# Kernel optimization log

Measured on AMD Instinct MI355X. Metric: run time of the kernel, lower is better.

Reference implementation:

```python
import jax, jax.numpy as jnp
import numpy as np

P_CLASSES = 1024   # num_classes_per_batch
K_SAMP = 4         # num_samples_per_class
MARGIN = 1.0
EPS = 1e-6
EMBED_DIM = 128


def setup_inputs() -> dict:
    key = jax.random.key(0)
    x = jax.random.normal(key, (P_CLASSES * K_SAMP, EMBED_DIM), dtype=jnp.float32)
    return {"x": x}


def reference(x):
    p, k = P_CLASSES, K_SAMP
    n = p * k
    # pairwise distances D[i,j] = sqrt(relu(|xi|^2 - 2 xi.xj + |xj|^2) + eps)
    norms = jnp.sum(x * x, axis=1)
    D = norms[:, None] - 2.0 * (x @ x.T) + norms[None, :]
    D = jnp.sqrt(jax.nn.relu(D) + EPS)  # [n, n]

    # all positive pairs (i<j) within each class, vectorized over classes
    ii, jj = np.triu_indices(k, 1)                      # [m], m = k*(k-1)/2
    c = np.arange(p)
    ri = (c[:, None] * k + ii[None, :]).reshape(-1)     # [P] = [p*m]
    rj = (c[:, None] * k + jj[None, :]).reshape(-1)
    pair_cls = np.repeat(c, len(ii))                    # class of each pair
    col_cls = np.arange(n) // k                         # class of each column
    neg_mask = jnp.asarray(pair_cls[:, None] != col_cls[None, :])  # [P, n]

    # masked logsumexp over negatives from both anchor rows (concat of the
    # two sliced rows in the original code)
    rows = jnp.concatenate([D[ri], D[rj]], axis=1)                 # [P, 2n]
    mask2 = jnp.concatenate([neg_mask, neg_mask], axis=1)
    vals = jnp.where(mask2, MARGIN - rows, -jnp.inf)
    lse = jax.scipy.special.logsumexp(vals, axis=1)                # [P]

    J = lse + D[ri, rj]
    return jnp.mean(jnp.square(jax.nn.relu(J))) / 2.0
```

## Files before the change

kernel.cpp:

```cpp
#include <hip/hip_runtime.h>

#define NROWS 4096
#define DIM 128
#define PCLS 1024
#define NPAIR 6144
#define MARGIN 1.0f
#define EPS 1e-6f
#define LOG2E 1.4426950408889634f
#define NSPLIT 16

typedef __attribute__((ext_vector_type(8))) short bf16x8;
typedef __attribute__((ext_vector_type(4))) float f32x4;

union FragU { uint4 u; bf16x8 v; };

__device__ __forceinline__ unsigned short f2bf(float f) {
    unsigned int b = __float_as_uint(f);
    b = (b + 0x7FFFu + ((b >> 16) & 1u)) >> 16;
    return (unsigned short)b;
}
__device__ __forceinline__ float bf2f(unsigned short u) {
    return __uint_as_float((unsigned int)u << 16);
}

__global__ void prep_kernel(const float* __restrict__ x,
                            unsigned short* __restrict__ xbf,
                            float* __restrict__ norms) {
    int row = blockIdx.x * 4 + (threadIdx.x >> 6);
    int l = threadIdx.x & 63;
    float2 v = *reinterpret_cast<const float2*>(x + row * DIM + 2 * l);
    unsigned int packed = (unsigned int)f2bf(v.x) | ((unsigned int)f2bf(v.y) << 16);
    *reinterpret_cast<unsigned int*>(xbf + row * DIM + 2 * l) = packed;
    float s = v.x * v.x + v.y * v.y;
    #pragma unroll
    for (int m = 1; m < 64; m <<= 1) s += __shfl_xor(s, m, 64);
    if (l == 0) norms[row] = s;
}

__launch_bounds__(512, 4)
__global__ void main_kernel(const unsigned short* __restrict__ xbf,
                            const float* __restrict__ norms,
                            unsigned short* __restrict__ partial,
                            float* __restrict__ posD) {
    __shared__ __align__(16) unsigned short lds[256 * DIM];
    const int t = threadIdx.x;
    const int w = t >> 6;
    const int l = t & 63;
    const int rb = blockIdx.x >> 4;
    const int cs = blockIdx.x & 15;
    const int rbase = rb * 128 + w * 16;
    const int cbase = cs * 256;
    const int lg = l >> 4;
    const int lr = l & 15;

    FragU afr[4];
    const char* abase = (const char*)xbf + (size_t)(rbase + lr) * 256 + lg * 16;
    #pragma unroll
    for (int s = 0; s < 4; ++s)
        afr[s].u = *reinterpret_cast<const uint4*>(abase + s * 64);

    float njv[16];
    #pragma unroll
    for (int tile = 0; tile < 16; ++tile)
        njv[tile] = norms[cbase + tile * 16 + lr];

    float ni[4];
    #pragma unroll
    for (int rr = 0; rr < 4; ++rr)
        ni[rr] = norms[rbase + lg * 4 + rr] + EPS;

    #pragma unroll
    for (int it = 0; it < 8; ++it) {
        int lin = it * 8192 + t * 16;
        int col = lin >> 8;
        int inner = lin & 255;
        uint4 v = *reinterpret_cast<const uint4*>(
            (const char*)xbf + (size_t)(cbase + col) * 256 + inner);
        *reinterpret_cast<uint4*>(
            (char*)lds + col * 256 + (inner ^ ((col & 7) << 4))) = v;
    }

    __syncthreads();

    float accS[4] = {0.f, 0.f, 0.f, 0.f};

    #pragma unroll
    for (int tile = 0; tile < 16; ++tile) {
        const int lcol = tile * 16 + lr;
        const float nj = njv[tile];
        const char* bbase = (const char*)lds + lcol * 256;
        const int xr = (lcol & 7) << 4;
        f32x4 acc = {0.f, 0.f, 0.f, 0.f};
        #pragma unroll
        for (int s = 0; s < 4; ++s) {
            FragU bu;
            int inner = s * 64 + lg * 16;
            bu.u = *reinterpret_cast<const uint4*>(bbase + (inner ^ xr));
            acc = __builtin_amdgcn_mfma_f32_16x16x32_bf16(afr[s].v, bu.v, acc, 0, 0, 0);
        }
        const bool diag = (cbase + tile * 16) == rbase;
        if (!diag) {
            #pragma unroll
            for (int rr = 0; rr < 4; ++rr) {
                float nn = ni[rr] + nj;
                float d2 = fmaf(-2.0f, acc[rr], nn);
                float d = __builtin_amdgcn_sqrtf(fmaxf(d2, EPS));
                accS[rr] += __builtin_amdgcn_exp2f(fmaf(d, -LOG2E, LOG2E));
            }
        } else {
            #pragma unroll
            for (int rr = 0; rr < 4; ++rr) {
                int a = lg * 4 + rr;
                int b = lr;
                float nn = ni[rr] + nj;
                float d2 = fmaf(-2.0f, acc[rr], nn);
                float d = __builtin_amdgcn_sqrtf(fmaxf(d2, EPS));
                float e = __builtin_amdgcn_exp2f(fmaf(d, -LOG2E, LOG2E));
                bool same = (a >> 2) == (b >> 2);
                accS[rr] += same ? 0.f : e;
                if (same && a < b) {
                    int i = a & 3, j = b & 3;
                    int idx = i * (7 - i) / 2 + (j - i - 1);
                    int cls = (rbase + a) >> 2;
                    posD[cls * 6 + idx] = d;
                }
            }
        }
    }
    #pragma unroll
    for (int rr = 0; rr < 4; ++rr) {
        #pragma unroll
        for (int m = 1; m < 16; m <<= 1) accS[rr] += __shfl_xor(accS[rr], m, 64);
    }
    if (lr == 0) {
        #pragma unroll
        for (int rr = 0; rr < 4; ++rr)
            partial[cs * NROWS + rbase + lg * 4 + rr] = f2bf(accS[rr]);
    }
}

__global__ void tail_kernel(const unsigned short* __restrict__ partial,
                            const float* __restrict__ posD,
                            float* __restrict__ out) {
    const int c = threadIdx.x;
    float S[4] = {0.f, 0.f, 0.f, 0.f};
    #pragma unroll
    for (int sp = 0; sp < NSPLIT; ++sp) {
        ushort4 v = *reinterpret_cast<const ushort4*>(partial + sp * NROWS + 4 * c);
        S[0] += bf2f(v.x); S[1] += bf2f(v.y); S[2] += bf2f(v.z); S[3] += bf2f(v.w);
    }
    const int II[6] = {0, 0, 0, 1, 1, 2};
    const int JJ[6] = {1, 2, 3, 2, 3, 3};
    float acc = 0.f;
    #pragma unroll
    for (int p = 0; p < 6; ++p) {
        float d = posD[c * 6 + p];
        float J = __logf(S[II[p]] + S[JJ[p]]) + d;
        float r = fmaxf(J, 0.f);
        acc += r * r;
    }
    #pragma unroll
    for (int m = 1; m < 64; m <<= 1) acc += __shfl_xor(acc, m, 64);
    __shared__ float red[16];
    if ((c & 63) == 0) red[c >> 6] = acc;
    __syncthreads();
    if (c < 64) {
        float v = (c < 16) ? red[c] : 0.f;
        #pragma unroll
        for (int m = 1; m < 16; m <<= 1) v += __shfl_xor(v, m, 64);
        if (c == 0) out[0] = v * (1.0f / (2.0f * (float)NPAIR));
    }
}

extern "C" void kernel_launch(void* const* d_in, const int* in_sizes, int n_in,
                              void* d_out, int out_size, void* d_ws, size_t ws_size,
                              hipStream_t stream) {
    const float* x = (const float*)d_in[0];
    char* ws = (char*)d_ws;
    unsigned short* xbf = (unsigned short*)ws;
    float* norms = (float*)(ws + 1048576);
    unsigned short* partial = (unsigned short*)(ws + 1048576 + 16384);
    float* posD = (float*)(ws + 1048576 + 16384 + 131072);
    float* out = (float*)d_out;

    hipLaunchKernelGGL(prep_kernel, dim3(NROWS / 4), dim3(256), 0, stream, x, xbf, norms);
    hipLaunchKernelGGL(main_kernel, dim3(512), dim3(512), 0, stream, xbf, norms, partial, posD);
    hipLaunchKernelGGL(tail_kernel, dim3(1), dim3(1024), 0, stream, partial, posD, out);
}
```

Measured before the change: 23.83 us.

## Fuse bf16 conversion and norm computation into main kernel, drop prep kernel

Removes the separate prep kernel and has each block of the main kernel read fp32 x directly, convert its row and column tiles to bf16 in registers/LDS, and compute row and column norms locally into shared arrays. This eliminates one kernel launch plus the write and reread of the bf16 copy and norms buffer. In exchange, each block redundantly converts and reduces its tiles, and it loads twice as many bytes per element from global memory (fp32 instead of bf16).

```diff
diff --git a/kernel.cpp b/kernel.cpp
--- a/kernel.cpp
+++ b/kernel.cpp
@@ -12,7 +12,7 @@
 typedef __attribute__((ext_vector_type(8))) short bf16x8;
 typedef __attribute__((ext_vector_type(4))) float f32x4;
 
-union FragU { uint4 u; bf16x8 v; };
+union FragU { uint4 u; bf16x8 v; unsigned short us[8]; };
 
 __device__ __forceinline__ unsigned short f2bf(float f) {
     unsigned int b = __float_as_uint(f);
@@ -23,26 +23,13 @@
     return __uint_as_float((unsigned int)u << 16);
 }
 
-__global__ void prep_kernel(const float* __restrict__ x,
-                            unsigned short* __restrict__ xbf,
-                            float* __restrict__ norms) {
-    int row = blockIdx.x * 4 + (threadIdx.x >> 6);
-    int l = threadIdx.x & 63;
-    float2 v = *reinterpret_cast<const float2*>(x + row * DIM + 2 * l);
-    unsigned int packed = (unsigned int)f2bf(v.x) | ((unsigned int)f2bf(v.y) << 16);
-    *reinterpret_cast<unsigned int*>(xbf + row * DIM + 2 * l) = packed;
-    float s = v.x * v.x + v.y * v.y;
-    #pragma unroll
-    for (int m = 1; m < 64; m <<= 1) s += __shfl_xor(s, m, 64);
-    if (l == 0) norms[row] = s;
-}
-
 __launch_bounds__(512, 4)
-__global__ void main_kernel(const unsigned short* __restrict__ xbf,
-                            const float* __restrict__ norms,
+__global__ void main_kernel(const float* __restrict__ x,
                             unsigned short* __restrict__ partial,
                             float* __restrict__ posD) {
     __shared__ __align__(16) unsigned short lds[256 * DIM];
+    __shared__ float normRow[128];
+    __shared__ float normCol[256];
     const int t = threadIdx.x;
     const int w = t >> 6;
     const int l = t & 63;
@@ -54,33 +41,62 @@
     const int lr = l & 15;
 
     FragU afr[4];
-    const char* abase = (const char*)xbf + (size_t)(rbase + lr) * 256 + lg * 16;
-    #pragma unroll
-    for (int s = 0; s < 4; ++s)
-        afr[s].u = *reinterpret_cast<const uint4*>(abase + s * 64);
+    float rn = 0.f;
+    const float* arow = x + (size_t)(rbase + lr) * DIM + lg * 8;
+    #pragma unroll
+    for (int s = 0; s < 4; ++s) {
+        float4 a0 = *reinterpret_cast<const float4*>(arow + s * 32);
+        float4 a1 = *reinterpret_cast<const float4*>(arow + s * 32 + 4);
+        afr[s].us[0] = f2bf(a0.x); afr[s].us[1] = f2bf(a0.y);
+        afr[s].us[2] = f2bf(a0.z); afr[s].us[3] = f2bf(a0.w);
+        afr[s].us[4] = f2bf(a1.x); afr[s].us[5] = f2bf(a1.y);
+        afr[s].us[6] = f2bf(a1.z); afr[s].us[7] = f2bf(a1.w);
+        rn = fmaf(a0.x, a0.x, rn); rn = fmaf(a0.y, a0.y, rn);
+        rn = fmaf(a0.z, a0.z, rn); rn = fmaf(a0.w, a0.w, rn);
+        rn = fmaf(a1.x, a1.x, rn); rn = fmaf(a1.y, a1.y, rn);
+        rn = fmaf(a1.z, a1.z, rn); rn = fmaf(a1.w, a1.w, rn);
+    }
+    rn += __shfl_xor(rn, 16, 64);
+    rn += __shfl_xor(rn, 32, 64);
+    if (lg == 0) normRow[w * 16 + lr] = rn;
+
+    #pragma unroll
+    for (int q = 0; q < 8; ++q) {
+        int col = q * 32 + (t >> 4);
+        int if32 = (t & 15) * 8;
+        const float* bp = x + (size_t)(cbase + col) * DIM + if32;
+        float4 b0 = *reinterpret_cast<const float4*>(bp);
+        float4 b1 = *reinterpret_cast<const float4*>(bp + 4);
+        FragU h;
+        h.us[0] = f2bf(b0.x); h.us[1] = f2bf(b0.y);
+        h.us[2] = f2bf(b0.z); h.us[3] = f2bf(b0.w);
+        h.us[4] = f2bf(b1.x); h.us[5] = f2bf(b1.y);
+        h.us[6] = f2bf(b1.z); h.us[7] = f2bf(b1.w);
+        int ib = if32 * 2;
+        *reinterpret_cast<uint4*>(
+            (char*)lds + col * 256 + (ib ^ ((col & 7) << 4))) = h.u;
+        float cn = 0.f;
+        cn = fmaf(b0.x, b0.x, cn); cn = fmaf(b0.y, b0.y, cn);
+        cn = fmaf(b0.z, b0.z, cn); cn = fmaf(b0.w, b0.w, cn);
+        cn = fmaf(b1.x, b1.x, cn); cn = fmaf(b1.y, b1.y, cn);
+        cn = fmaf(b1.z, b1.z, cn); cn = fmaf(b1.w, b1.w, cn);
+        cn += __shfl_xor(cn, 1, 64);
+        cn += __shfl_xor(cn, 2, 64);
+        cn += __shfl_xor(cn, 4, 64);
+        cn += __shfl_xor(cn, 8, 64);
+        if ((t & 15) == 0) normCol[col] = cn;
+    }
+
+    __syncthreads();
 
     float njv[16];
     #pragma unroll
     for (int tile = 0; tile < 16; ++tile)
-        njv[tile] = norms[cbase + tile * 16 + lr];
-
+        njv[tile] = normCol[tile * 16 + lr];
     float ni[4];
     #pragma unroll
     for (int rr = 0; rr < 4; ++rr)
-        ni[rr] = norms[rbase + lg * 4 + rr] + EPS;
-
-    #pragma unroll
-    for (int it = 0; it < 8; ++it) {
-        int lin = it * 8192 + t * 16;
-        int col = lin >> 8;
-        int inner = lin & 255;
-        uint4 v = *reinterpret_cast<const uint4*>(
-            (const char*)xbf + (size_t)(cbase + col) * 256 + inner);
-        *reinterpret_cast<uint4*>(
-            (char*)lds + col * 256 + (inner ^ ((col & 7) << 4))) = v;
-    }
-
-    __syncthreads();
+        ni[rr] = normRow[w * 16 + lg * 4 + rr] + EPS;
 
     float accS[4] = {0.f, 0.f, 0.f, 0.f};
 
@@ -177,13 +193,10 @@
                               hipStream_t stream) {
     const float* x = (const float*)d_in[0];
     char* ws = (char*)d_ws;
-    unsigned short* xbf = (unsigned short*)ws;
-    float* norms = (float*)(ws + 1048576);
-    unsigned short* partial = (unsigned short*)(ws + 1048576 + 16384);
-    float* posD = (float*)(ws + 1048576 + 16384 + 131072);
+    unsigned short* partial = (unsigned short*)ws;
+    float* posD = (float*)(ws + 131072);
     float* out = (float*)d_out;
 
-    hipLaunchKernelGGL(prep_kernel, dim3(NROWS / 4), dim3(256), 0, stream, x, xbf, norms);
-    hipLaunchKernelGGL(main_kernel, dim3(512), dim3(512), 0, stream, xbf, norms, partial, posD);
+    hipLaunchKernelGGL(main_kernel, dim3(512), dim3(512), 0, stream, x, partial, posD);
     hipLaunchKernelGGL(tail_kernel, dim3(1), dim3(1024), 0, stream, partial, posD, out);
 }
```

New measurement: 23.35 us (median of 2 runs). 2.0% less time.
